# Performance work log

Measured on AMD Instinct MI355X. Metric: run time of the kernel, lower is better.

Reference implementation:

```python
import jax, jax.numpy as jnp
import numpy as np

# Static CT geometry (ctlib-style): parallel-beam pixel-driven backprojection
VIEWS, DETS = 512, 512   # sinogram: angles x detector bins
H, W = 256, 256          # reconstructed image grid


def setup_inputs() -> dict:
    key = jax.random.key(0)
    proj = jax.random.normal(key, (4, 1, VIEWS, DETS), dtype=jnp.float32)
    # options = [dImg (pixel size), dDet (detector bin size), Ang0, dAng]
    options = jnp.array([1.0, 1.5, 0.0, np.pi / VIEWS], dtype=jnp.float32)
    return {"proj": proj, "options": options}


def reference(proj, options):
    # proj: [B, 1, VIEWS, DETS] sinogram; returns image [B, 1, H, W]
    dImg, dDet, ang0, dAng = options[0], options[1], options[2], options[3]

    ang = ang0 + dAng * jnp.arange(VIEWS, dtype=jnp.float32)          # [V]
    cos_a, sin_a = jnp.cos(ang), jnp.sin(ang)
    # pixel-center world coordinates (y axis points up)
    xs = (jnp.arange(W, dtype=jnp.float32) - (W - 1) / 2.0) * dImg     # [W]
    ys = ((H - 1) / 2.0 - jnp.arange(H, dtype=jnp.float32)) * dImg     # [H]

    # signed distance of each pixel to the detector axis for each view: t[v,y,x]
    t = cos_a[:, None, None] * xs[None, None, :] + sin_a[:, None, None] * ys[None, :, None]
    u = t / dDet + (DETS - 1) / 2.0                                    # fractional detector coord

    i0 = jnp.floor(u)
    w = u - i0                                                         # linear interp weight
    i0i = i0.astype(jnp.int32)
    i1i = i0i + 1
    m0 = ((i0i >= 0) & (i0i < DETS)).astype(proj.dtype)
    m1 = ((i1i >= 0) & (i1i < DETS)).astype(proj.dtype)
    i0c = jnp.clip(i0i, 0, DETS - 1)
    i1c = jnp.clip(i1i, 0, DETS - 1)

    p = proj[:, 0]                                                     # [B, V, D]
    vix = jnp.arange(VIEWS)[:, None, None]                             # [V,1,1]
    p0 = p[:, vix, i0c]                                                # [B, V, H, W]
    p1 = p[:, vix, i1c]
    val = p0 * ((1.0 - w) * m0) + p1 * (w * m1)                        # interpolated ray values

    img = dAng * jnp.sum(val, axis=1)                                  # accumulate over views
    return img[:, None, :, :]
```

## Files before the change

### kernel.cpp

```cpp
#include <hip/hip_runtime.h>
#include <math.h>

#define VIEWS  512
#define DETS   512
#define HH     256
#define WW     256
#define VSPLIT 4
#define VCHUNK (VIEWS / VSPLIT)
#define TS     32
#define CV     16
#define WIN    48
#define NCHUNK (VCHUNK / CV)

__global__ __launch_bounds__(256) void backproj_kernel(
    const float* __restrict__ proj,
    const float* __restrict__ options,
    float* __restrict__ out)
{
    __shared__ float2 s_cs[VCHUNK];
    __shared__ float  s_w0f[CV];
    __shared__ float  s_win[CV][WIN];

    const float dImg = options[0];
    const float dDet = options[1];
    const float ang0 = options[2];
    const float dAng = options[3];

    const int tid = threadIdx.x;
    const int blk = blockIdx.x;
    const int vq  = blk & 3;
    const int tx  = (blk >> 2) & 7;
    const int ty  = (blk >> 5) & 7;
    const int b   = blk >> 8;
    const int v0  = vq * VCHUNK;
    const int x0t = tx * TS;
    const int y0t = ty * TS;

    if (tid < VCHUNK) {
        float a = ang0 + dAng * (float)(v0 + tid);
        float ss, cc;
        sincosf(a, &ss, &cc);
        s_cs[tid] = make_float2(cc, ss);
    }
    __syncthreads();

    const float sc   = dImg / dDet;
    const float uoff = (DETS - 1) * 0.5f;

    const int xl = tid & 31;
    const int yg = tid >> 5;
    const float xs = ((float)(x0t + xl) - (WW - 1) * 0.5f) * sc;
    float ys[4];
#pragma unroll
    for (int k = 0; k < 4; ++k)
        ys[k] = ((HH - 1) * 0.5f - (float)(y0t + yg * 4 + k)) * sc;

    const float xa = ((float)x0t - (WW - 1) * 0.5f) * sc;
    const float xb = ((float)(x0t + TS - 1) - (WW - 1) * 0.5f) * sc;
    const float ya = ((HH - 1) * 0.5f - (float)y0t) * sc;
    const float yb = ((HH - 1) * 0.5f - (float)(y0t + TS - 1)) * sc;

    const int sv = tid >> 4;
    const int sj = tid & 15;

    float acc[4] = {0.f, 0.f, 0.f, 0.f};

    for (int ch = 0; ch < NCHUNK; ++ch) {
        {
            float2 cs = s_cs[ch * CV + sv];
            float umin = fminf(cs.x * xa, cs.x * xb)
                       + fminf(cs.y * ya, cs.y * yb) + uoff;
            int w0 = (int)floorf(umin) - 2;
            if (sj == 0) s_w0f[sv] = (float)w0;
            const float* row =
                proj + ((size_t)((b * VIEWS) + v0 + ch * CV + sv) * DETS) + w0;
            s_win[sv][sj]      = row[sj];
            s_win[sv][sj + 16] = row[sj + 16];
            s_win[sv][sj + 32] = row[sj + 32];
        }
        __syncthreads();

#pragma unroll 4
        for (int vv = 0; vv < CV; ++vv) {
            float2 cs = s_cs[ch * CV + vv];
            float tb  = fmaf(cs.x, xs, uoff - s_w0f[vv]);
            const float* win = s_win[vv];
#pragma unroll
            for (int k = 0; k < 4; ++k) {
                float u = fmaf(cs.y, ys[k], tb);
                int   i = (int)u;
                float w = u - (float)i;
                float p0 = win[i];
                float p1 = win[i + 1];
                acc[k] = fmaf(w, p1 - p0, acc[k] + p0);
            }
        }
        __syncthreads();
    }

    float* o = out + ((size_t)b * HH + (y0t + yg * 4)) * WW + x0t + xl;
#pragma unroll
    for (int k = 0; k < 4; ++k)
        atomicAdd(o + (size_t)k * WW, acc[k] * dAng);
}

extern "C" void kernel_launch(void* const* d_in, const int* in_sizes, int n_in,
                              void* d_out, int out_size, void* d_ws, size_t ws_size,
                              hipStream_t stream) {
    const float* proj    = (const float*)d_in[0];
    const float* options = (const float*)d_in[1];
    float* out = (float*)d_out;

    hipMemsetAsync(d_out, 0, (size_t)out_size * sizeof(float), stream);

    dim3 grid(4 * 64 * VSPLIT);
    dim3 block(256);
    backproj_kernel<<<grid, block, 0, stream>>>(proj, options, out);
}
```

Measured before the change: 89.04 us.

## Double-buffer projection windows with register prefetch and split views further

Projection window rows for the next chunk of views are loaded into registers while the current chunk is interpolated, then written to an alternate shared buffer, so each chunk needs one barrier instead of two. Per-view cos, sin and offset are packed into a float4 to cut shared loads. The view split doubles to 8, which doubles the block count and the atomic adds on the output, and launch bounds now ask for 8 blocks per CU. The interpolation weight uses the hardware fract builtin, and the added shared memory and register pressure could limit occupancy.

New measurement: 85.47 us. 1.04x faster.

```diff
diff --git a/kernel.cpp b/kernel.cpp
--- a/kernel.cpp
+++ b/kernel.cpp
@@ -5,21 +5,21 @@
 #define DETS   512
 #define HH     256
 #define WW     256
-#define VSPLIT 4
+#define VSPLIT 8
 #define VCHUNK (VIEWS / VSPLIT)
 #define TS     32
 #define CV     16
 #define WIN    48
 #define NCHUNK (VCHUNK / CV)
 
-__global__ __launch_bounds__(256) void backproj_kernel(
+__global__ __launch_bounds__(256, 8) void backproj_kernel(
     const float* __restrict__ proj,
     const float* __restrict__ options,
     float* __restrict__ out)
 {
     __shared__ float2 s_cs[VCHUNK];
-    __shared__ float  s_w0f[CV];
-    __shared__ float  s_win[CV][WIN];
+    __shared__ float4 s_pk[2][CV];
+    __shared__ float  s_win[2][CV][WIN];
 
     const float dImg = options[0];
     const float dDet = options[1];
@@ -28,10 +28,10 @@
 
     const int tid = threadIdx.x;
     const int blk = blockIdx.x;
-    const int vq  = blk & 3;
-    const int tx  = (blk >> 2) & 7;
-    const int ty  = (blk >> 5) & 7;
-    const int b   = blk >> 8;
+    const int vq  = blk & 7;
+    const int tx  = (blk >> 3) & 7;
+    const int ty  = (blk >> 6) & 7;
+    const int b   = blk >> 9;
     const int v0  = vq * VCHUNK;
     const int x0t = tx * TS;
     const int y0t = ty * TS;
@@ -42,7 +42,6 @@
         sincosf(a, &ss, &cc);
         s_cs[tid] = make_float2(cc, ss);
     }
-    __syncthreads();
 
     const float sc   = dImg / dDet;
     const float uoff = (DETS - 1) * 0.5f;
@@ -62,40 +61,64 @@
 
     const int sv = tid >> 4;
     const int sj = tid & 15;
+    const float* __restrict__ pbase = proj + (size_t)(b * VIEWS + v0) * DETS;
+
+    __syncthreads();
+
+    float t0, t1, t2, cR, sR, w0f;
+    {
+        float2 cs = s_cs[sv];
+        cR = cs.x; sR = cs.y;
+        float umin = fminf(cR * xa, cR * xb) + fminf(sR * ya, sR * yb) + uoff;
+        w0f = floorf(umin) - 2.0f;
+        const float* row = pbase + (size_t)sv * DETS + (int)w0f;
+        t0 = row[sj]; t1 = row[sj + 16]; t2 = row[sj + 32];
+    }
+    s_win[0][sv][sj]      = t0;
+    s_win[0][sv][sj + 16] = t1;
+    s_win[0][sv][sj + 32] = t2;
+    if (sj == 0) s_pk[0][sv] = make_float4(cR, sR, uoff - w0f, 0.0f);
+    __syncthreads();
 
     float acc[4] = {0.f, 0.f, 0.f, 0.f};
 
     for (int ch = 0; ch < NCHUNK; ++ch) {
-        {
-            float2 cs = s_cs[ch * CV + sv];
-            float umin = fminf(cs.x * xa, cs.x * xb)
-                       + fminf(cs.y * ya, cs.y * yb) + uoff;
-            int w0 = (int)floorf(umin) - 2;
-            if (sj == 0) s_w0f[sv] = (float)w0;
-            const float* row =
-                proj + ((size_t)((b * VIEWS) + v0 + ch * CV + sv) * DETS) + w0;
-            s_win[sv][sj]      = row[sj];
-            s_win[sv][sj + 16] = row[sj + 16];
-            s_win[sv][sj + 32] = row[sj + 32];
+        const int cur = ch & 1;
+        const int nxt = cur ^ 1;
+
+        if (ch + 1 < NCHUNK) {
+            int gv = (ch + 1) * CV + sv;
+            float2 cs = s_cs[gv];
+            cR = cs.x; sR = cs.y;
+            float umin = fminf(cR * xa, cR * xb) + fminf(sR * ya, sR * yb) + uoff;
+            w0f = floorf(umin) - 2.0f;
+            const float* row = pbase + (size_t)gv * DETS + (int)w0f;
+            t0 = row[sj]; t1 = row[sj + 16]; t2 = row[sj + 32];
         }
-        __syncthreads();
 
 #pragma unroll 4
         for (int vv = 0; vv < CV; ++vv) {
-            float2 cs = s_cs[ch * CV + vv];
-            float tb  = fmaf(cs.x, xs, uoff - s_w0f[vv]);
-            const float* win = s_win[vv];
+            float4 pk = s_pk[cur][vv];
+            float tb  = fmaf(pk.x, xs, pk.z);
+            const float* win = s_win[cur][vv];
 #pragma unroll
             for (int k = 0; k < 4; ++k) {
-                float u = fmaf(cs.y, ys[k], tb);
+                float u = fmaf(pk.y, ys[k], tb);
                 int   i = (int)u;
-                float w = u - (float)i;
+                float w = __builtin_amdgcn_fractf(u);
                 float p0 = win[i];
                 float p1 = win[i + 1];
                 acc[k] = fmaf(w, p1 - p0, acc[k] + p0);
             }
         }
-        __syncthreads();
+
+        if (ch + 1 < NCHUNK) {
+            s_win[nxt][sv][sj]      = t0;
+            s_win[nxt][sv][sj + 16] = t1;
+            s_win[nxt][sv][sj + 32] = t2;
+            if (sj == 0) s_pk[nxt][sv] = make_float4(cR, sR, uoff - w0f, 0.0f);
+            __syncthreads();
+        }
     }
 
     float* o = out + ((size_t)b * HH + (y0t + yg * 4)) * WW + x0t + xl;
```
